# Optimization experiments

Measured on AMD Instinct MI355X. Metric: run time of the kernel, lower is better.

The kernel has to match this reference:

```python
import jax, jax.numpy as jnp
import numpy as np

D, P, H, FF, HD = 1024, 512, 16, 4096, 64
B, L = 2, 1024
EPS = 1e-5


def rotate_half(x):
    x1, x2 = jnp.split(x, 2, axis=-1)
    return jnp.concatenate([-x2, x1], axis=-1)


def apply_rope(x, pos):  # x: [B,H,L,HD], pos: [L,HD] angles
    c = jnp.cos(pos)[None, None]
    s = jnp.sin(pos)[None, None]
    return x * c + rotate_half(x) * s


def layer_norm(x, g, b):
    mu = jnp.mean(x, axis=-1, keepdims=True)
    var = jnp.var(x, axis=-1, keepdims=True)
    return (x - mu) * jax.lax.rsqrt(var + EPS) * g + b


def heads(x):  # [B,L,D] -> [B,H,L,HD]
    Bq, Lq, _ = x.shape
    return x.reshape(Bq, Lq, H, HD).transpose(0, 2, 1, 3)


def attention(q, k, v, alibi, pos, mask):
    if pos is not None:
        q = apply_rope(q, pos)
        k = apply_rope(k, pos)
    scores = jnp.einsum('bhqd,bhkd->bhqk', q, k) * (HD ** -0.5)
    scores = jnp.where(mask[:, None, None, :], -jnp.inf, scores)
    scores = scores + alibi[None]
    w = jax.nn.softmax(scores, axis=-1)
    out = jnp.einsum('bhqk,bhkd->bhqd', w, v)
    return out.transpose(0, 2, 1, 3).reshape(out.shape[0], out.shape[2], D)


def setup_inputs() -> dict:
    key = jax.random.key(0)
    ks = iter(jax.random.split(key, 64))

    def rn(shape, scale=1.0):
        return jax.random.normal(next(ks), shape, dtype=jnp.float32) * scale

    inp = {
        'memory': rn((B, L, D)),
        'tgt': rn((B, L, D)),
        'self_alibi_bias': rn((H, L, L)),
        'self_pos_emb': rn((L, HD)),
        'cross_alibi_bias': rn((H, L, L)),
        'cross_pos_emb': rn((L, HD)),
        'mask': jax.random.randint(next(ks), (B, L), 0, 2) > 0,
        # self attention params
        'sa_lat_w': rn((D, P), 0.02), 'sa_lat_b': jnp.zeros((P,)),
        'sa_q_w': rn((P, D), 0.02), 'sa_q_b': jnp.zeros((D,)),
        'sa_k_w': rn((P, D), 0.02), 'sa_k_b': jnp.zeros((D,)),
        'sa_v_w': rn((P, D), 0.02), 'sa_v_b': jnp.zeros((D,)),
        'sa_out_w': rn((D, D), 0.02), 'sa_out_b': jnp.zeros((D,)),
        # cross attention params
        'ca_lat_w': rn((D, P), 0.02), 'ca_lat_b': jnp.zeros((P,)),
        'ca_q_w': rn((D, D), 0.02), 'ca_q_b': jnp.zeros((D,)),
        'ca_k_w': rn((P, D), 0.02), 'ca_k_b': jnp.zeros((D,)),
        'ca_v_w': rn((P, D), 0.02), 'ca_v_b': jnp.zeros((D,)),
        'ca_out_w': rn((D, D), 0.02), 'ca_out_b': jnp.zeros((D,)),
        # ffn + norms
        'lin1_w': rn((D, FF), 0.02), 'lin1_b': jnp.zeros((FF,)),
        'lin2_w': rn((FF, D), 0.02), 'lin2_b': jnp.zeros((D,)),
        'n1_g': jnp.ones((D,)), 'n1_b': jnp.zeros((D,)),
        'n2_g': jnp.ones((D,)), 'n2_b': jnp.zeros((D,)),
        'n3_g': jnp.ones((D,)), 'n3_b': jnp.zeros((D,)),
    }
    return inp


def reference(memory, tgt, self_alibi_bias, self_pos_emb, cross_alibi_bias,
              cross_pos_emb, mask,
              sa_lat_w, sa_lat_b, sa_q_w, sa_q_b, sa_k_w, sa_k_b,
              sa_v_w, sa_v_b, sa_out_w, sa_out_b,
              ca_lat_w, ca_lat_b, ca_q_w, ca_q_b, ca_k_w, ca_k_b,
              ca_v_w, ca_v_b, ca_out_w, ca_out_b,
              lin1_w, lin1_b, lin2_w, lin2_b,
              n1_g, n1_b, n2_g, n2_b, n3_g, n3_b):
    # self attention (q,k,v all from latent projection of tgt)
    proj = tgt @ sa_lat_w + sa_lat_b                      # [B,L,P]
    q = heads(proj @ sa_q_w + sa_q_b)
    k = heads(proj @ sa_k_w + sa_k_b)
    v = heads(proj @ sa_v_w + sa_v_b)
    sa = attention(q, k, v, self_alibi_bias, self_pos_emb, mask)
    sa = sa @ sa_out_w + sa_out_b
    x = tgt + layer_norm(sa, n1_g, n1_b)

    # cross attention (q from current tgt stream, k/v from latent of memory)
    mproj = memory @ ca_lat_w + ca_lat_b                  # [B,L,P]
    q = heads(x @ ca_q_w + ca_q_b)
    k = heads(mproj @ ca_k_w + ca_k_b)
    v = heads(mproj @ ca_v_w + ca_v_b)
    ca = attention(q, k, v, cross_alibi_bias, cross_pos_emb, mask)
    ca = ca @ ca_out_w + ca_out_b
    x = x + layer_norm(ca, n2_g, n2_b)

    # FFN
    f = jax.nn.gelu(x @ lin1_w + lin1_b, approximate=False) @ lin2_w + lin2_b
    x = layer_norm(x + f, n3_g, n3_b)
    return x
```

## Files before the change

kernel.cpp:

```cpp
#include <hip/hip_runtime.h>
#include <hip/hip_bf16.h>
#include <math.h>

typedef __hip_bfloat16 hbf16;
typedef __attribute__((ext_vector_type(8))) short bf16x8;
typedef __attribute__((ext_vector_type(4))) float f32x4;

constexpr int kD  = 1024;
constexpr int kP  = 512;
constexpr int kH  = 16;
constexpr int kFF = 4096;
constexpr int kHD = 64;
constexpr int kB  = 2;
constexpr int kL  = 1024;
constexpr int kTok = kB * kL;

__device__ inline short f2bf(float x) { hbf16 h = __float2bfloat16(x); return *(short*)&h; }

__global__ __launch_bounds__(256) void transpose_bf16(
    const float* __restrict__ src, short* __restrict__ dst, int K, int N)
{
    __shared__ float t[32][33];
    int n0 = blockIdx.x * 32, k0 = blockIdx.y * 32;
    int tx = threadIdx.x & 31, ty = threadIdx.x >> 5;
    #pragma unroll
    for (int r = ty; r < 32; r += 8)
        t[r][tx] = src[(size_t)(k0 + r) * N + n0 + tx];
    __syncthreads();
    #pragma unroll
    for (int r = ty; r < 32; r += 8)
        dst[(size_t)(n0 + r) * K + k0 + tx] = f2bf(t[tx][r]);
}

__global__ __launch_bounds__(256) void bias_fill(
    const float* __restrict__ bias, float* __restrict__ C, int N, int total4)
{
    int i = blockIdx.x * 256 + threadIdx.x;
    if (i >= total4) return;
    int n = (i * 4) & (N - 1);
    *(float4*)&C[(size_t)i * 4] = *(const float4*)&bias[n];
}

__global__ void concat_bias(float* __restrict__ o, const float* __restrict__ a,
                            const float* __restrict__ b, const float* __restrict__ c, int n)
{
    int i = blockIdx.x * blockDim.x + threadIdx.x;
    if (i < n) o[i] = a[i];
    else if (i < 2 * n) { if (b) o[i] = b[i - n]; }
    else if (i < 3 * n) { if (c) o[i] = c[i - 2 * n]; }
}

constexpr int LDK = 40;
__global__ __launch_bounds__(256) void gemm_mfma(
    const float* __restrict__ A, const short* __restrict__ WT,
    const float* __restrict__ bias, float* __restrict__ C,
    int M, int N, int K, int act, int ksplit)
{
    __shared__ short As[128 * LDK];
    __shared__ short Bs[128 * LDK];
    const int tid = threadIdx.x;
    const int m0 = blockIdx.y * 128, n0 = blockIdx.x * 128;
    const int ks = K / ksplit;
    const int kbeg = blockIdx.z * ks, kend = kbeg + ks;
    const int wave = tid >> 6, lane = tid & 63;
    const int wm = (wave & 1) * 64, wn = (wave >> 1) * 64;
    const int l15 = lane & 15, quad = lane >> 4;

    const int am = tid >> 3, akq = (tid & 7) * 4;
    const int bn = tid >> 2, bkg = (tid & 3) * 8;

    f32x4 acc[4][4];
    #pragma unroll
    for (int i = 0; i < 4; ++i)
        #pragma unroll
        for (int j = 0; j < 4; ++j)
            acc[i][j] = (f32x4){0.f, 0.f, 0.f, 0.f};

    float4 ra[4];
    bf16x8 rb[2];
    #pragma unroll
    for (int e = 0; e < 4; ++e)
        ra[e] = *(const float4*)&A[(size_t)(m0 + am + e * 32) * K + kbeg + akq];
    #pragma unroll
    for (int e = 0; e < 2; ++e)
        rb[e] = *(const bf16x8*)&WT[(size_t)(n0 + bn + e * 64) * K + kbeg + bkg];

    for (int kk = kbeg; kk < kend; kk += 32) {
        #pragma unroll
        for (int e = 0; e < 4; ++e) {
            short4 s4 = make_short4(f2bf(ra[e].x), f2bf(ra[e].y), f2bf(ra[e].z), f2bf(ra[e].w));
            *(short4*)&As[(am + e * 32) * LDK + akq] = s4;
        }
        #pragma unroll
        for (int e = 0; e < 2; ++e)
            *(bf16x8*)&Bs[(bn + e * 64) * LDK + bkg] = rb[e];
        __syncthreads();

        if (kk + 32 < kend) {
            #pragma unroll
            for (int e = 0; e < 4; ++e)
                ra[e] = *(const float4*)&A[(size_t)(m0 + am + e * 32) * K + kk + 32 + akq];
            #pragma unroll
            for (int e = 0; e < 2; ++e)
                rb[e] = *(const bf16x8*)&WT[(size_t)(n0 + bn + e * 64) * K + kk + 32 + bkg];
        }

        bf16x8 af[4], bfr[4];
        #pragma unroll
        for (int i = 0; i < 4; ++i)
            af[i] = *(bf16x8*)&As[(wm + i * 16 + l15) * LDK + quad * 8];
        #pragma unroll
        for (int j = 0; j < 4; ++j)
            bfr[j] = *(bf16x8*)&Bs[(wn + j * 16 + l15) * LDK + quad * 8];
        #pragma unroll
        for (int i = 0; i < 4; ++i)
            #pragma unroll
            for (int j = 0; j < 4; ++j)
                acc[i][j] = __builtin_amdgcn_mfma_f32_16x16x32_bf16(af[i], bfr[j], acc[i][j], 0, 0, 0);
        __syncthreads();
    }

    #pragma unroll
    for (int j = 0; j < 4; ++j) {
        int n = n0 + wn + j * 16 + l15;
        if (ksplit == 1) {
            float bv = bias[n];
            #pragma unroll
            for (int i = 0; i < 4; ++i) {
                int mb = m0 + wm + i * 16 + quad * 4;
                #pragma unroll
                for (int r = 0; r < 4; ++r) {
                    float v = acc[i][j][r] + bv;
                    if (act) v = v * 0.5f * (1.0f + erff(v * 0.70710678118654752f));
                    C[(size_t)(mb + r) * N + n] = v;
                }
            }
        } else {
            #pragma unroll
            for (int i = 0; i < 4; ++i) {
                int mb = m0 + wm + i * 16 + quad * 4;
                #pragma unroll
                for (int r = 0; r < 4; ++r)
                    atomicAdd(&C[(size_t)(mb + r) * N + n], acc[i][j][r]);
            }
        }
    }
}

__global__ void qk_pack(const float* __restrict__ x, const float* __restrict__ pos,
                        short* __restrict__ outp, float scale, int ldx, int off)
{
    int idx = blockIdx.x * blockDim.x + threadIdx.x;
    if (idx >= kTok * kH * 32) return;
    int d = idx & 31;
    int h = (idx >> 5) & (kH - 1);
    int row = idx >> 9;
    int l = row & (kL - 1);
    int b = row >> 10;
    float a1 = pos[l * kHD + d];
    float a2 = pos[l * kHD + d + 32];
    size_t base = (size_t)row * ldx + off + h * kHD;
    float x1 = x[base + d], x2 = x[base + d + 32];
    float r1 = (x1 * cosf(a1) - x2 * sinf(a1)) * scale;
    float r2 = (x2 * cosf(a2) + x1 * sinf(a2)) * scale;
    size_t ob = ((size_t)(b * kH + h) * kL + l) * 64;
    outp[ob + d]      = f2bf(r1);
    outp[ob + d + 32] = f2bf(r2);
}

__global__ __launch_bounds__(256) void v_pack(const float* __restrict__ v, short* __restrict__ outp,
                                              int ldx, int off)
{
    int l0 = blockIdx.x * 64, h = blockIdx.y, b = blockIdx.z;
    __shared__ float t[64][65];
    int tid = threadIdx.x;
    #pragma unroll
    for (int e = 0; e < 4; ++e) {
        int idx = tid + e * 256;
        int r = idx >> 4, c4 = (idx & 15) * 4;
        const float4 vv = *(const float4*)&v[(size_t)(b * kL + l0 + r) * ldx + off + h * kHD + c4];
        t[r][c4] = vv.x; t[r][c4 + 1] = vv.y; t[r][c4 + 2] = vv.z; t[r][c4 + 3] = vv.w;
    }
    __syncthreads();
    int hd = tid >> 2, seg = (tid & 3) * 16;
    size_t ob = ((size_t)(b * kH + h) * 64 + hd) * kL + l0 + seg;
    short tmp[16];
    #pragma unroll
    for (int i = 0; i < 16; ++i) tmp[i] = f2bf(t[seg + i][hd]);
    #pragma unroll
    for (int i = 0; i < 16; i += 4)
        *(short4*)&outp[ob + i] = make_short4(tmp[i], tmp[i + 1], tmp[i + 2], tmp[i + 3]);
}

constexpr int AQ = 64, AK = 64;
__global__ __launch_bounds__(256, 2) void attn_mfma(
    const short* __restrict__ qpk, const short* __restrict__ kpk,
    const short* __restrict__ vpk, const float* __restrict__ alibi,
    const int* __restrict__ mask, float* __restrict__ out)
{
    const int q0 = blockIdx.x * AQ, h = blockIdx.y, b = blockIdx.z;
    const int tid = threadIdx.x, wave = tid >> 6, lane = tid & 63;
    const int l15 = lane & 15, quad = lane >> 4;
    __shared__ short Qf[4096];
    __shared__ short Kf[4096];
    __shared__ short Vf[4096];
    __shared__ float ALPS[4 * 1088];

    const short* qbase = qpk + ((size_t)(b * kH + h) * kL) * 64;
    const short* kbase = kpk + ((size_t)(b * kH + h) * kL) * 64;
    const short* vbase = vpk + ((size_t)(b * kH + h) * 64) * kL;
    const float* abase = alibi + ((size_t)h * kL + q0) * kL;
    const int*   mbase = mask + b * kL;

    const int sr = tid >> 3, sc8 = (tid & 7) * 8;
    const int sQuad = (sc8 >> 3) & 3, sS = sc8 >> 5;
    const int ar = tid >> 4, ac4 = (tid & 15) * 4;

    #pragma unroll
    for (int e = 0; e < 2; ++e) {
        int r = sr + e * 32;
        int slot = ((r >> 4) * 2 + sS) * 512 + (r & 15) * 32 + sQuad * 8;
        *(bf16x8*)&Qf[slot] = *(const bf16x8*)&qbase[(size_t)(q0 + r) * 64 + sc8];
    }

    bf16x8 rk[2], rv[2];
    float4 ral[4];
    int4 rmk;
    auto load_tile = [&](int k0) {
        #pragma unroll
        for (int e = 0; e < 2; ++e) {
            int r = sr + e * 32;
            rk[e] = *(const bf16x8*)&kbase[(size_t)(k0 + r) * 64 + sc8];
            rv[e] = *(const bf16x8*)&vbase[(size_t)r * kL + k0 + sc8];
        }
        #pragma unroll
        for (int e = 0; e < 4; ++e)
            ral[e] = *(const float4*)&abase[(size_t)(ar + e * 16) * kL + k0 + ac4];
        rmk = *(const int4*)&mbase[k0 + ac4];
    };
    auto store_tile = [&]() {
        #pragma unroll
        for (int e = 0; e < 2; ++e) {
            int r = sr + e * 32;
            int slot = ((r >> 4) * 2 + sS) * 512 + (r & 15) * 32 + sQuad * 8;
            *(bf16x8*)&Kf[slot] = rk[e];
            *(bf16x8*)&Vf[slot] = rv[e];
        }
        #pragma unroll
        for (int e = 0; e < 4; ++e) {
            float4 a = ral[e];
            a.x = rmk.x ? -1e30f : a.x;
            a.y = rmk.y ? -1e30f : a.y;
            a.z = rmk.z ? -1e30f : a.z;
            a.w = rmk.w ? -1e30f : a.w;
            *(float4*)&ALPS[(ar + e * 16) * 68 + ac4] = a;
        }
    };

    float mst[4], lst[4];
    #pragma unroll
    for (int r = 0; r < 4; ++r) { mst[r] = -3e38f; lst[r] = 0.f; }
    f32x4 oacc[4];
    #pragma unroll
    for (int j = 0; j < 4; ++j) oacc[j] = (f32x4){0.f, 0.f, 0.f, 0.f};

    load_tile(0);
    __syncthreads();

    bf16x8 aq[2];
    #pragma unroll
    for (int s = 0; s < 2; ++s)
        aq[s] = *(bf16x8*)&Qf[(wave * 2 + s) * 512 + l15 * 32 + quad * 8];

    for (int t = 0; t < kL / AK; ++t) {
        store_tile();
        __syncthreads();
        if (t + 1 < kL / AK) load_tile((t + 1) * AK);

        f32x4 sacc[4];
        #pragma unroll
        for (int nt = 0; nt < 4; ++nt) sacc[nt] = (f32x4){0.f, 0.f, 0.f, 0.f};
        #pragma unroll
        for (int nt = 0; nt < 4; ++nt)
            #pragma unroll
            for (int s = 0; s < 2; ++s) {
                bf16x8 bk = *(bf16x8*)&Kf[(nt * 2 + s) * 512 + l15 * 32 + quad * 8];
                sacc[nt] = __builtin_amdgcn_mfma_f32_16x16x32_bf16(aq[s], bk, sacc[nt], 0, 0, 0);
            }

        float sv[4][4];
        float mx[4] = {-3e38f, -3e38f, -3e38f, -3e38f};
        #pragma unroll
        for (int nt = 0; nt < 4; ++nt)
            #pragma unroll
            for (int r = 0; r < 4; ++r) {
                float al = ALPS[(wave * 16 + quad * 4 + r) * 68 + nt * 16 + l15];
                float s = sacc[nt][r] + al;
                sv[nt][r] = s;
                mx[r] = fmaxf(mx[r], s);
            }
        #pragma unroll
        for (int m = 1; m <= 8; m <<= 1)
            #pragma unroll
            for (int r = 0; r < 4; ++r)
                mx[r] = fmaxf(mx[r], __shfl_xor(mx[r], m));
        float alpha[4], lsum[4];
        #pragma unroll
        for (int r = 0; r < 4; ++r) {
            float mn = fmaxf(mst[r], mx[r]);
            alpha[r] = __expf(mst[r] - mn);
            mst[r] = mn;
            lsum[r] = 0.f;
        }
        #pragma unroll
        for (int nt = 0; nt < 4; ++nt)
            #pragma unroll
            for (int r = 0; r < 4; ++r) {
                float p = __expf(sv[nt][r] - mst[r]);
                sv[nt][r] = p;
                lsum[r] += p;
            }
        #pragma unroll
        for (int m = 1; m <= 8; m <<= 1)
            #pragma unroll
            for (int r = 0; r < 4; ++r)
                lsum[r] += __shfl_xor(lsum[r], m);
        #pragma unroll
        for (int r = 0; r < 4; ++r) lst[r] = lst[r] * alpha[r] + lsum[r];

        #pragma unroll
        for (int nt = 0; nt < 4; ++nt)
            #pragma unroll
            for (int r = 0; r < 4; ++r)
                ALPS[wave * 1088 + (quad * 4 + r) * 67 + nt * 16 + l15] = sv[nt][r];
        #pragma unroll
        for (int j = 0; j < 4; ++j)
            #pragma unroll
            for (int r = 0; r < 4; ++r)
                oacc[j][r] *= alpha[r];

        #pragma unroll
        for (int s = 0; s < 2; ++s) {
            int pb = wave * 1088 + l15 * 67 + s * 32 + quad * 8;
            bf16x8 ap;
            #pragma unroll
            for (int e = 0; e < 8; ++e) ap[e] = f2bf(ALPS[pb + e]);
            #pragma unroll
            for (int j = 0; j < 4; ++j) {
                bf16x8 bv = *(bf16x8*)&Vf[(j * 2 + s) * 512 + l15 * 32 + quad * 8];
                oacc[j] = __builtin_amdgcn_mfma_f32_16x16x32_bf16(ap, bv, oacc[j], 0, 0, 0);
            }
        }
        __syncthreads();
    }

    #pragma unroll
    for (int j = 0; j < 4; ++j)
        #pragma unroll
        for (int r = 0; r < 4; ++r) {
            int qrow = q0 + wave * 16 + quad * 4 + r;
            out[(size_t)(b * kL + qrow) * kD + h * kHD + j * 16 + l15] = oacc[j][r] / lst[r];
        }
}

__global__ __launch_bounds__(256) void add_ln(
    const float* __restrict__ res, const float* __restrict__ z,
    const float* __restrict__ g, const float* __restrict__ bi,
    float* __restrict__ out)
{
    int row = blockIdx.x, tid = threadIdx.x;
    __shared__ float red[256], red2[256];
    const float* zr = z + (size_t)row * kD;
    float s = 0.f, sq = 0.f;
    for (int i = tid; i < kD; i += 256) { float vv = zr[i]; s += vv; sq += vv * vv; }
    red[tid] = s; red2[tid] = sq; __syncthreads();
    for (int st = 128; st > 0; st >>= 1) {
        if (tid < st) { red[tid] += red[tid + st]; red2[tid] += red2[tid + st]; }
        __syncthreads();
    }
    float mean = red[0] / kD;
    float var = red2[0] / kD - mean * mean;
    float rstd = rsqrtf(var + 1e-5f);
    for (int i = tid; i < kD; i += 256) {
        float vv = (zr[i] - mean) * rstd * g[i] + bi[i];
        out[(size_t)row * kD + i] = res[(size_t)row * kD + i] + vv;
    }
}

__global__ __launch_bounds__(256) void ln_final(
    const float* __restrict__ res, const float* __restrict__ f,
    const float* __restrict__ g, const float* __restrict__ bi,
    float* __restrict__ out)
{
    int row = blockIdx.x, tid = threadIdx.x;
    __shared__ float tt[kD];
    __shared__ float red[256], red2[256];
    float s = 0.f, sq = 0.f;
    for (int i = tid; i < kD; i += 256) {
        float vv = res[(size_t)row * kD + i] + f[(size_t)row * kD + i];
        tt[i] = vv; s += vv; sq += vv * vv;
    }
    red[tid] = s; red2[tid] = sq; __syncthreads();
    for (int st = 128; st > 0; st >>= 1) {
        if (tid < st) { red[tid] += red[tid + st]; red2[tid] += red2[tid + st]; }
        __syncthreads();
    }
    float mean = red[0] / kD;
    float var = red2[0] / kD - mean * mean;
    float rstd = rsqrtf(var + 1e-5f);
    for (int i = tid; i < kD; i += 256)
        out[(size_t)row * kD + i] = (tt[i] - mean) * rstd * g[i] + bi[i];
}

extern "C" void kernel_launch(void* const* d_in, const int* in_sizes, int n_in,
                              void* d_out, int out_size, void* d_ws, size_t ws_size,
                              hipStream_t stream)
{
    const float* memory      = (const float*)d_in[0];
    const float* tgt         = (const float*)d_in[1];
    const float* self_alibi  = (const float*)d_in[2];
    const float* self_pos    = (const float*)d_in[3];
    const float* cross_alibi = (const float*)d_in[4];
    const float* cross_pos   = (const float*)d_in[5];
    const int*   mask        = (const int*)d_in[6];
    const float* sa_lat_w = (const float*)d_in[7];   const float* sa_lat_b = (const float*)d_in[8];
    const float* sa_q_w   = (const float*)d_in[9];   const float* sa_q_b   = (const float*)d_in[10];
    const float* sa_k_w   = (const float*)d_in[11];  const float* sa_k_b   = (const float*)d_in[12];
    const float* sa_v_w   = (const float*)d_in[13];  const float* sa_v_b   = (const float*)d_in[14];
    const float* sa_out_w = (const float*)d_in[15];  const float* sa_out_b = (const float*)d_in[16];
    const float* ca_lat_w = (const float*)d_in[17];  const float* ca_lat_b = (const float*)d_in[18];
    const float* ca_q_w   = (const float*)d_in[19];  const float* ca_q_b   = (const float*)d_in[20];
    const float* ca_k_w   = (const float*)d_in[21];  const float* ca_k_b   = (const float*)d_in[22];
    const float* ca_v_w   = (const float*)d_in[23];  const float* ca_v_b   = (const float*)d_in[24];
    const float* ca_out_w = (const float*)d_in[25];  const float* ca_out_b = (const float*)d_in[26];
    const float* lin1_w   = (const float*)d_in[27];  const float* lin1_b   = (const float*)d_in[28];
    const float* lin2_w   = (const float*)d_in[29];  const float* lin2_b   = (const float*)d_in[30];
    const float* n1_g = (const float*)d_in[31];  const float* n1_b = (const float*)d_in[32];
    const float* n2_g = (const float*)d_in[33];  const float* n2_b = (const float*)d_in[34];
    const float* n3_g = (const float*)d_in[35];  const float* n3_b = (const float*)d_in[36];

    const size_t M1 = 1u << 20;
    float* W     = (float*)d_ws;
    float* xb    = W + 0 * M1;
    float* tmp   = W + 2 * M1;
    float* proj  = W + 4 * M1;
    float* qkvb  = W + 5 * M1;
    float* attnb = W + 11 * M1;
    float* ffh   = W + 4 * M1;
    short* wslot = (short*)(W + 13 * M1);
    float* bcat  = W + 11 * M1;
    short* qpk = (short*)(W + 2 * M1);
    short* kpk = (short*)(W + 3 * M1);
    short* vpk = (short*)(W + 4 * M1);

    auto gemm = [&](const float* A, const float* Wt, const float* bias, float* C,
                    int M, int N, int K, int act, int S) {
        transpose_bf16<<<dim3(N / 32, K / 32), dim3(256), 0, stream>>>(Wt, wslot, K, N);
        if (S > 1)
            bias_fill<<<dim3(M * N / 1024), dim3(256), 0, stream>>>(bias, C, N, M * N / 4);
        gemm_mfma<<<dim3(N / 128, M / 128, S), dim3(256), 0, stream>>>(A, wslot, bias, C, M, N, K, act, S);
    };
    dim3 agrid(kL / AQ, kH, kB);
    dim3 vgrid(kL / 64, kH, kB);
    dim3 tgD(kD / 32, kP / 32);

    gemm(tgt, sa_lat_w, sa_lat_b, proj, kTok, kP, kD, 0, 4);
    transpose_bf16<<<tgD, dim3(256), 0, stream>>>(sa_q_w, wslot, kP, kD);
    transpose_bf16<<<tgD, dim3(256), 0, stream>>>(sa_k_w, wslot + (size_t)kD * kP, kP, kD);
    transpose_bf16<<<tgD, dim3(256), 0, stream>>>(sa_v_w, wslot + (size_t)2 * kD * kP, kP, kD);
    concat_bias<<<dim3(12), dim3(256), 0, stream>>>(bcat, sa_q_b, sa_k_b, sa_v_b, kD);
    gemm_mfma<<<dim3(3 * kD / 128, kTok / 128, 1), dim3(256), 0, stream>>>(
        proj, wslot, bcat, qkvb, kTok, 3 * kD, kP, 0, 1);
    qk_pack<<<dim3(4096), dim3(256), 0, stream>>>(qkvb, self_pos, qpk, 0.125f, 3 * kD, 0);
    qk_pack<<<dim3(4096), dim3(256), 0, stream>>>(qkvb, self_pos, kpk, 1.0f, 3 * kD, kD);
    v_pack<<<vgrid, dim3(256), 0, stream>>>(qkvb, vpk, 3 * kD, 2 * kD);
    attn_mfma<<<agrid, dim3(256), 0, stream>>>(qpk, kpk, vpk, self_alibi, mask, attnb);
    gemm(attnb, sa_out_w, sa_out_b, tmp, kTok, kD, kD, 0, 2);
    add_ln<<<dim3(kTok), dim3(256), 0, stream>>>(tgt, tmp, n1_g, n1_b, xb);

    gemm(memory, ca_lat_w, ca_lat_b, proj, kTok, kP, kD, 0, 4);
    gemm(xb, ca_q_w, ca_q_b, qkvb, kTok, kD, kD, 0, 2);
    transpose_bf16<<<tgD, dim3(256), 0, stream>>>(ca_k_w, wslot, kP, kD);
    transpose_bf16<<<tgD, dim3(256), 0, stream>>>(ca_v_w, wslot + (size_t)kD * kP, kP, kD);
    concat_bias<<<dim3(8), dim3(256), 0, stream>>>(bcat, ca_k_b, ca_v_b, nullptr, kD);
    float* kvb = qkvb + 2 * M1;
    gemm_mfma<<<dim3(2 * kD / 128, kTok / 128, 1), dim3(256), 0, stream>>>(
        proj, wslot, bcat, kvb, kTok, 2 * kD, kP, 0, 1);
    qk_pack<<<dim3(4096), dim3(256), 0, stream>>>(qkvb, cross_pos, qpk, 0.125f, kD, 0);
    qk_pack<<<dim3(4096), dim3(256), 0, stream>>>(kvb, cross_pos, kpk, 1.0f, 2 * kD, 0);
    v_pack<<<vgrid, dim3(256), 0, stream>>>(kvb, vpk, 2 * kD, kD);
    attn_mfma<<<agrid, dim3(256), 0, stream>>>(qpk, kpk, vpk, cross_alibi, mask, attnb);
    gemm(attnb, ca_out_w, ca_out_b, tmp, kTok, kD, kD, 0, 2);
    add_ln<<<dim3(kTok), dim3(256), 0, stream>>>(xb, tmp, n2_g, n2_b, xb);

    gemm(xb, lin1_w, lin1_b, ffh, kTok, kFF, kD, 1, 1);
    gemm(ffh, lin2_w, lin2_b, tmp, kTok, kD, kFF, 0, 4);
    ln_final<<<dim3(kTok), dim3(256), 0, stream>>>(xb, tmp, n3_g, n3_b, (float*)d_out);
}
```

Measured before the change: 673.8 us.

## Use bf16 activations end to end with direct global-to-LDS loads in GEMM

GEMM operands become bf16 activations, produced by new cast kernels or emitted as bf16 directly by attention, layernorm and the FFN1 epilogue. This halves A-operand traffic and removes the in-kernel fp32-to-bf16 conversion. The GEMM now stages tiles through global_load_lds with an unpadded LDS layout, which drops the register prefetch double-buffer and may introduce bank conflicts. It also adds an XCD-aware workgroup swizzle for L2 locality, at the cost of extra cast kernels and a reshuffled workspace layout.

New measurement: 693.7 us. 1.03x slower.

```diff
diff --git a/kernel.cpp b/kernel.cpp
--- a/kernel.cpp
+++ b/kernel.cpp
@@ -17,6 +17,21 @@
 
 __device__ inline short f2bf(float x) { hbf16 h = __float2bfloat16(x); return *(short*)&h; }
 
+__device__ __forceinline__ void gload16(const void* g, void* l) {
+    __builtin_amdgcn_global_load_lds(
+        (const __attribute__((address_space(1))) void*)g,
+        (__attribute__((address_space(3))) void*)l, 16, 0, 0);
+}
+
+__global__ __launch_bounds__(256) void cast_bf16(
+    const float* __restrict__ in, short* __restrict__ out, int total4)
+{
+    int i = blockIdx.x * 256 + threadIdx.x;
+    if (i >= total4) return;
+    float4 v = *(const float4*)&in[(size_t)i * 4];
+    *(short4*)&out[(size_t)i * 4] = make_short4(f2bf(v.x), f2bf(v.y), f2bf(v.z), f2bf(v.w));
+}
+
 __global__ __launch_bounds__(256) void transpose_bf16(
     const float* __restrict__ src, short* __restrict__ dst, int K, int N)
 {
@@ -50,24 +65,32 @@
     else if (i < 3 * n) { if (c) o[i] = c[i - 2 * n]; }
 }
 
-constexpr int LDK = 40;
 __global__ __launch_bounds__(256) void gemm_mfma(
-    const float* __restrict__ A, const short* __restrict__ WT,
-    const float* __restrict__ bias, float* __restrict__ C,
+    const short* __restrict__ A, const short* __restrict__ WT,
+    const float* __restrict__ bias, float* __restrict__ C, short* __restrict__ C16,
     int M, int N, int K, int act, int ksplit)
 {
-    __shared__ short As[128 * LDK];
-    __shared__ short Bs[128 * LDK];
+    __shared__ short As[128 * 32];
+    __shared__ short Bs[128 * 32];
     const int tid = threadIdx.x;
-    const int m0 = blockIdx.y * 128, n0 = blockIdx.x * 128;
+
+    const int gx = gridDim.x;
+    const int nwg = gx * gridDim.y;
+    const int orig = blockIdx.y * gx + blockIdx.x;
+    const int qq = nwg >> 3, rr = nwg & 7;
+    const int xcd = orig & 7, lid = orig >> 3;
+    const int swz = (xcd < rr) ? (xcd * (qq + 1) + lid)
+                               : (rr * (qq + 1) + (xcd - rr) * qq + lid);
+    const int m0 = (swz / gx) * 128, n0 = (swz % gx) * 128;
+
     const int ks = K / ksplit;
     const int kbeg = blockIdx.z * ks, kend = kbeg + ks;
     const int wave = tid >> 6, lane = tid & 63;
+    const int l15 = lane & 15, quad = lane >> 4;
     const int wm = (wave & 1) * 64, wn = (wave >> 1) * 64;
-    const int l15 = lane & 15, quad = lane >> 4;
-
-    const int am = tid >> 3, akq = (tid & 7) * 4;
-    const int bn = tid >> 2, bkg = (tid & 3) * 8;
+
+    const int srow = wave * 32 + (lane >> 2);
+    const int scol = (lane & 3) * 8;
 
     f32x4 acc[4][4];
     #pragma unroll
@@ -76,42 +99,20 @@
         for (int j = 0; j < 4; ++j)
             acc[i][j] = (f32x4){0.f, 0.f, 0.f, 0.f};
 
-    float4 ra[4];
-    bf16x8 rb[2];
-    #pragma unroll
-    for (int e = 0; e < 4; ++e)
-        ra[e] = *(const float4*)&A[(size_t)(m0 + am + e * 32) * K + kbeg + akq];
-    #pragma unroll
-    for (int e = 0; e < 2; ++e)
-        rb[e] = *(const bf16x8*)&WT[(size_t)(n0 + bn + e * 64) * K + kbeg + bkg];
-
     for (int kk = kbeg; kk < kend; kk += 32) {
-        #pragma unroll
-        for (int e = 0; e < 4; ++e) {
-            short4 s4 = make_short4(f2bf(ra[e].x), f2bf(ra[e].y), f2bf(ra[e].z), f2bf(ra[e].w));
-            *(short4*)&As[(am + e * 32) * LDK + akq] = s4;
-        }
-        #pragma unroll
-        for (int e = 0; e < 2; ++e)
-            *(bf16x8*)&Bs[(bn + e * 64) * LDK + bkg] = rb[e];
+        gload16(&A [(size_t)(m0 + srow) * K + kk + scol],      &As[wave * 1024]);
+        gload16(&A [(size_t)(m0 + srow + 16) * K + kk + scol], &As[wave * 1024 + 512]);
+        gload16(&WT[(size_t)(n0 + srow) * K + kk + scol],      &Bs[wave * 1024]);
+        gload16(&WT[(size_t)(n0 + srow + 16) * K + kk + scol], &Bs[wave * 1024 + 512]);
         __syncthreads();
 
-        if (kk + 32 < kend) {
-            #pragma unroll
-            for (int e = 0; e < 4; ++e)
-                ra[e] = *(const float4*)&A[(size_t)(m0 + am + e * 32) * K + kk + 32 + akq];
-            #pragma unroll
-            for (int e = 0; e < 2; ++e)
-                rb[e] = *(const bf16x8*)&WT[(size_t)(n0 + bn + e * 64) * K + kk + 32 + bkg];
-        }
-
         bf16x8 af[4], bfr[4];
         #pragma unroll
         for (int i = 0; i < 4; ++i)
-            af[i] = *(bf16x8*)&As[(wm + i * 16 + l15) * LDK + quad * 8];
+            af[i] = *(bf16x8*)&As[(wm + i * 16 + l15) * 32 + quad * 8];
         #pragma unroll
         for (int j = 0; j < 4; ++j)
-            bfr[j] = *(bf16x8*)&Bs[(wn + j * 16 + l15) * LDK + quad * 8];
+            bfr[j] = *(bf16x8*)&Bs[(wn + j * 16 + l15) * 32 + quad * 8];
         #pragma unroll
         for (int i = 0; i < 4; ++i)
             #pragma unroll
@@ -132,7 +133,8 @@
                 for (int r = 0; r < 4; ++r) {
                     float v = acc[i][j][r] + bv;
                     if (act) v = v * 0.5f * (1.0f + erff(v * 0.70710678118654752f));
-                    C[(size_t)(mb + r) * N + n] = v;
+                    if (C)   C[(size_t)(mb + r) * N + n] = v;
+                    if (C16) C16[(size_t)(mb + r) * N + n] = f2bf(v);
                 }
             }
         } else {
@@ -196,7 +198,7 @@
 __global__ __launch_bounds__(256, 2) void attn_mfma(
     const short* __restrict__ qpk, const short* __restrict__ kpk,
     const short* __restrict__ vpk, const float* __restrict__ alibi,
-    const int* __restrict__ mask, float* __restrict__ out)
+    const int* __restrict__ mask, short* __restrict__ out)
 {
     const int q0 = blockIdx.x * AQ, h = blockIdx.y, b = blockIdx.z;
     const int tid = threadIdx.x, wave = tid >> 6, lane = tid & 63;
@@ -359,14 +361,14 @@
         #pragma unroll
         for (int r = 0; r < 4; ++r) {
             int qrow = q0 + wave * 16 + quad * 4 + r;
-            out[(size_t)(b * kL + qrow) * kD + h * kHD + j * 16 + l15] = oacc[j][r] / lst[r];
+            out[(size_t)(b * kL + qrow) * kD + h * kHD + j * 16 + l15] = f2bf(oacc[j][r] / lst[r]);
         }
 }
 
 __global__ __launch_bounds__(256) void add_ln(
     const float* __restrict__ res, const float* __restrict__ z,
     const float* __restrict__ g, const float* __restrict__ bi,
-    float* __restrict__ out)
+    float* __restrict__ out, short* __restrict__ out16)
 {
     int row = blockIdx.x, tid = threadIdx.x;
     __shared__ float red[256], red2[256];
@@ -383,7 +385,9 @@
     float rstd = rsqrtf(var + 1e-5f);
     for (int i = tid; i < kD; i += 256) {
         float vv = (zr[i] - mean) * rstd * g[i] + bi[i];
-        out[(size_t)row * kD + i] = res[(size_t)row * kD + i] + vv;
+        float o = res[(size_t)row * kD + i] + vv;
+        out[(size_t)row * kD + i] = o;
+        out16[(size_t)row * kD + i] = f2bf(o);
     }
 }
 
@@ -440,60 +444,69 @@
     const float* n3_g = (const float*)d_in[35];  const float* n3_b = (const float*)d_in[36];
 
     const size_t M1 = 1u << 20;
-    float* W     = (float*)d_ws;
-    float* xb    = W + 0 * M1;
-    float* tmp   = W + 2 * M1;
-    float* proj  = W + 4 * M1;
-    float* qkvb  = W + 5 * M1;
-    float* attnb = W + 11 * M1;
-    float* ffh   = W + 4 * M1;
-    short* wslot = (short*)(W + 13 * M1);
-    float* bcat  = W + 11 * M1;
-    short* qpk = (short*)(W + 2 * M1);
-    short* kpk = (short*)(W + 3 * M1);
-    short* vpk = (short*)(W + 4 * M1);
-
-    auto gemm = [&](const float* A, const float* Wt, const float* bias, float* C,
+    float* W      = (float*)d_ws;
+    float* xb     = W;
+    short* tgt16  = (short*)W;
+    float* tmp    = W + 2 * M1;
+    short* mem16  = (short*)(W + 2 * M1);
+    short* xb16   = (short*)(W + 4 * M1);
+    float* proj   = W + 5 * M1;
+    short* qpk    = (short*)(W + 5 * M1);
+    short* proj16 = (short*)(W + 6 * M1);
+    float* qkvb   = W + 6 * M1 + M1 / 2;
+    short* attnb16= (short*)(W + 6 * M1 + M1 / 2);
+    short* ffh16  = (short*)(W + 7 * M1 + M1 / 2);
+    short* wslot  = (short*)(W + 12 * M1 + M1 / 2);
+    short* kpk    = (short*)(W + 12 * M1 + M1 / 2);
+    short* vpk    = (short*)(W + 13 * M1 + M1 / 2);
+    float* bcat   = W + 14 * M1 + M1 / 2;
+
+    auto gemm = [&](const short* A, const float* Wt, const float* bias, float* C, short* C16,
                     int M, int N, int K, int act, int S) {
         transpose_bf16<<<dim3(N / 32, K / 32), dim3(256), 0, stream>>>(Wt, wslot, K, N);
         if (S > 1)
             bias_fill<<<dim3(M * N / 1024), dim3(256), 0, stream>>>(bias, C, N, M * N / 4);
-        gemm_mfma<<<dim3(N / 128, M / 128, S), dim3(256), 0, stream>>>(A, wslot, bias, C, M, N, K, act, S);
+        gemm_mfma<<<dim3(N / 128, M / 128, S), dim3(256), 0, stream>>>(A, wslot, bias, C, C16, M, N, K, act, S);
     };
     dim3 agrid(kL / AQ, kH, kB);
     dim3 vgrid(kL / 64, kH, kB);
     dim3 tgD(kD / 32, kP / 32);
 
-    gemm(tgt, sa_lat_w, sa_lat_b, proj, kTok, kP, kD, 0, 4);
+    cast_bf16<<<dim3(2048), dim3(256), 0, stream>>>(tgt, tgt16, kTok * kD / 4);
+    gemm(tgt16, sa_lat_w, sa_lat_b, proj, nullptr, kTok, kP, kD, 0, 4);
+    cast_bf16<<<dim3(1024), dim3(256), 0, stream>>>(proj, proj16, kTok * kP / 4);
     transpose_bf16<<<tgD, dim3(256), 0, stream>>>(sa_q_w, wslot, kP, kD);
     transpose_bf16<<<tgD, dim3(256), 0, stream>>>(sa_k_w, wslot + (size_t)kD * kP, kP, kD);
     transpose_bf16<<<tgD, dim3(256), 0, stream>>>(sa_v_w, wslot + (size_t)2 * kD * kP, kP, kD);
     concat_bias<<<dim3(12), dim3(256), 0, stream>>>(bcat, sa_q_b, sa_k_b, sa_v_b, kD);
     gemm_mfma<<<dim3(3 * kD / 128, kTok / 128, 1), dim3(256), 0, stream>>>(
-        proj, wslot, bcat, qkvb, kTok, 3 * kD, kP, 0, 1);
+        proj16, wslot, bcat, qkvb, nullptr, kTok, 3 * kD, kP, 0, 1);
     qk_pack<<<dim3(4096), dim3(256), 0, stream>>>(qkvb, self_pos, qpk, 0.125f, 3 * kD, 0);
     qk_pack<<<dim3(4096), dim3(256), 0, stream>>>(qkvb, self_pos, kpk, 1.0f, 3 * kD, kD);
     v_pack<<<vgrid, dim3(256), 0, stream>>>(qkvb, vpk, 3 * kD, 2 * kD);
-    attn_mfma<<<agrid, dim3(256), 0, stream>>>(qpk, kpk, vpk, self_alibi, mask, attnb);
-    gemm(attnb, sa_out_w, sa_out_b, tmp, kTok, kD, kD, 0, 2);
-    add_ln<<<dim3(kTok), dim3(256), 0, stream>>>(tgt, tmp, n1_g, n1_b, xb);
-
-    gemm(memory, ca_lat_w, ca_lat_b, proj, kTok, kP, kD, 0, 4);
-    gemm(xb, ca_q_w, ca_q_b, qkvb, kTok, kD, kD, 0, 2);
+    attn_mfma<<<agrid, dim3(256), 0, stream>>>(qpk, kpk, vpk, self_alibi, mask, attnb16);
+    gemm(attnb16, sa_out_w, sa_out_b, tmp, nullptr, kTok, kD, kD, 0, 2);
+    add_ln<<<dim3(kTok), dim3(256), 0, stream>>>(tgt, tmp, n1_g, n1_b, xb, xb16);
+
+    cast_bf16<<<dim3(2048), dim3(256), 0, stream>>>(memory, mem16, kTok * kD / 4);
+    gemm(mem16, ca_lat_w, ca_lat_b, proj, nullptr, kTok, kP, kD, 0, 4);
+    cast_bf16<<<dim3(1024), dim3(256), 0, stream>>>(proj, proj16, kTok * kP / 4);
+    float* qb  = qkvb;
+    float* kvb = qkvb + 2 * M1;
+    gemm(xb16, ca_q_w, ca_q_b, qb, nullptr, kTok, kD, kD, 0, 2);
     transpose_bf16<<<tgD, dim3(256), 0, stream>>>(ca_k_w, wslot, kP, kD);
     transpose_bf16<<<tgD, dim3(256), 0, stream>>>(ca_v_w, wslot + (size_t)kD * kP, kP, kD);
     concat_bias<<<dim3(8), dim3(256), 0, stream>>>(bcat, ca_k_b, ca_v_b, nullptr, kD);
-    float* kvb = qkvb + 2 * M1;
     gemm_mfma<<<dim3(2 * kD / 128, kTok / 128, 1), dim3(256), 0, stream>>>(
-        proj, wslot, bcat, kvb, kTok, 2 * kD, kP, 0, 1);
-    qk_pack<<<dim3(4096), dim3(256), 0, stream>>>(qkvb, cross_pos, qpk, 0.125f, kD, 0);
+        proj16, wslot, bcat, kvb, nullptr, kTok, 2 * kD, kP, 0, 1);
+    qk_pack<<<dim3(4096), dim3(256), 0, stream>>>(qb, cross_pos, qpk, 0.125f, kD, 0);
     qk_pack<<<dim3(4096), dim3(256), 0, stream>>>(kvb, cross_pos, kpk, 1.0f, 2 * kD, 0);
     v_pack<<<vgrid, dim3(256), 0, stream>>>(kvb, vpk, 2 * kD, kD);
-    attn_mfma<<<agrid, dim3(256), 0, stream>>>(qpk, kpk, vpk, cross_alibi, mask, attnb);
-    gemm(attnb, ca_out_w, ca_out_b, tmp, kTok, kD, kD, 0, 2);
-    add_ln<<<dim3(kTok), dim3(256), 0, stream>>>(xb, tmp, n2_g, n2_b, xb);
-
-    gemm(xb, lin1_w, lin1_b, ffh, kTok, kFF, kD, 1, 1);
-    gemm(ffh, lin2_w, lin2_b, tmp, kTok, kD, kFF, 0, 4);
+    attn_mfma<<<agrid, dim3(256), 0, stream>>>(qpk, kpk, vpk, cross_alibi, mask, attnb16);
+    gemm(attnb16, ca_out_w, ca_out_b, tmp, nullptr, kTok, kD, kD, 0, 2);
+    add_ln<<<dim3(kTok), dim3(256), 0, stream>>>(xb, tmp, n2_g, n2_b, xb, xb16);
+
+    gemm(xb16, lin1_w, lin1_b, nullptr, ffh16, kTok, kFF, kD, 1, 1);
+    gemm(ffh16, lin2_w, lin2_b, tmp, nullptr, kTok, kD, kFF, 0, 4);
     ln_final<<<dim3(kTok), dim3(256), 0, stream>>>(xb, tmp, n3_g, n3_b, (float*)d_out);
 }
```
